# Kernel tuning notes

Hardware: AMD Instinct MI355X
Metric: run time of the kernel (lower is better)

Reference implementation:

```python
import jax, jax.numpy as jnp
import numpy as np

N, D, H, E = 50000, 64, 4, 400000
LN_EPS = 1e-5


def setup_inputs() -> dict:
    key = jax.random.key(0)
    ks = jax.random.split(key, 8)
    x = jax.random.normal(ks[0], (N, D), dtype=jnp.float32)
    edge_index = jax.random.randint(ks[1], (2, E), 0, N, dtype=jnp.int64)
    # nn.Linear(dim, dim*heads, bias=False): weight shape (H*D, D)
    W_lin = jax.random.normal(ks[2], (H * D, D), dtype=jnp.float32) * (1.0 / np.sqrt(D))
    attn_src = jax.random.normal(ks[3], (H, D), dtype=jnp.float32) * 0.1
    attn_dst = jax.random.normal(ks[4], (H, D), dtype=jnp.float32) * 0.1
    # nn.Linear(dim*heads, dim): weight (D, H*D), bias (D,)
    W_out = jax.random.normal(ks[5], (D, H * D), dtype=jnp.float32) * (1.0 / np.sqrt(H * D))
    b_out = jnp.zeros((D,), dtype=jnp.float32)
    ln_g = jnp.ones((D,), dtype=jnp.float32)
    ln_b = jnp.zeros((D,), dtype=jnp.float32)
    return {"x": x, "edge_index": edge_index, "W_lin": W_lin,
            "attn_src": attn_src, "attn_dst": attn_dst,
            "W_out": W_out, "b_out": b_out, "ln_g": ln_g, "ln_b": ln_b}


def reference(x, edge_index, W_lin, attn_src, attn_dst, W_out, b_out, ln_g, ln_b):
    n = x.shape[0]
    i, j = edge_index[0], edge_index[1]  # dst, src node ids per edge
    xh = (x @ W_lin.T).reshape(n, H, D)                 # [N,H,D]
    # per-node attention contributions (equivalent to per-edge dot in source)
    s_dst = jnp.einsum('nhd,hd->nh', xh, attn_dst)      # [N,H]
    s_src = jnp.einsum('nhd,hd->nh', xh, attn_src)      # [N,H]
    alpha = jax.nn.leaky_relu(s_dst[i] + s_src[j], 0.2) # [E,H]
    alpha_exp = jnp.exp(alpha)                          # source uses raw exp (no max-shift)
    denom = jax.ops.segment_sum(alpha_exp, i, num_segments=n)  # [N,H]
    attn = alpha_exp / (denom[i] + 1e-9)                # [E,H]
    msg = attn[:, :, None] * xh[j]                      # [E,H,D]
    out = jax.ops.segment_sum(msg, i, num_segments=n)   # [N,H,D]
    out = out.reshape(n, H * D) @ W_out.T + b_out       # [N,D]
    y = jax.nn.elu(out) + x
    mu = jnp.mean(y, axis=-1, keepdims=True)
    var = jnp.mean(jnp.square(y - mu), axis=-1, keepdims=True)
    return (y - mu) * jax.lax.rsqrt(var + LN_EPS) * ln_g + ln_b
```

## Files before the change

### kernel.cpp

```cpp
#include <hip/hip_runtime.h>

#define N_NODES 50000
#define DIM     64
#define HEADS   4
#define NEDGES  400000
#define HD      256
#define MAXDEG  32
#define NTILES  3125

typedef _Float16 half4v __attribute__((ext_vector_type(4)));
typedef _Float16 half8v __attribute__((ext_vector_type(8)));
typedef float    f32x4  __attribute__((ext_vector_type(4)));

union EU { int2 i2; half4v h; };

__global__ __launch_bounds__(256) void k_wG(
    const float* __restrict__ W_lin,
    const float* __restrict__ attn_src,
    const float* __restrict__ attn_dst,
    const float* __restrict__ W_out,
    _Float16* __restrict__ G2T,
    float* __restrict__ weff,
    int* __restrict__ cnt)
{
    const int b = blockIdx.x;
    const int t = threadIdx.x;

    for (int idx = b * 256 + t; idx < N_NODES; idx += 65 * 256)
        cnt[idx] = 0;

    if (b < 64) {
        const int id = b * 256 + t;
        const int d = id >> 8, rem = id & 255, m = rem >> 2, h = rem & 3;
        float acc = 0.f;
        for (int k = 0; k < DIM; ++k)
            acc = fmaf(W_lin[(h * DIM + k) * DIM + m], W_out[d * HD + h * DIM + k], acc);
        G2T[d * HD + m * 4 + h] = (_Float16)acc;
    } else {
        for (int id = t; id < 512; id += 256) {
            const int sd = id >> 8, rem = id & 255, h = rem >> 6, k = rem & 63;
            const float* av = sd ? attn_dst : attn_src;
            float acc = 0.f;
            for (int d = 0; d < DIM; ++d)
                acc = fmaf(av[h * DIM + d], W_lin[(h * DIM + d) * DIM + k], acc);
            weff[(sd * 4 + h) * DIM + k] = acc;
        }
    }
}

__global__ __launch_bounds__(256) void k_xS(
    const float* __restrict__ x,
    const float* __restrict__ weff,
    _Float16* __restrict__ x16,
    float* __restrict__ S)
{
    const int t = threadIdx.x;
    const int base = blockIdx.x * 32;

    const int ni = base + (t >> 3);
    if (ni < N_NODES) {
        const int combo = t & 7;
        const float4* xr = (const float4*)(x + (size_t)ni * DIM);
        const float4* wr = (const float4*)(weff + combo * DIM);
        float acc = 0.f;
#pragma unroll
        for (int kp = 0; kp < 16; ++kp) {
            const float4 a = xr[kp], bw = wr[kp];
            acc = fmaf(a.x, bw.x, acc);
            acc = fmaf(a.y, bw.y, acc);
            acc = fmaf(a.z, bw.z, acc);
            acc = fmaf(a.w, bw.w, acc);
        }
        S[(size_t)ni * 8 + combo] = acc;
    }

    const size_t e0 = (size_t)base * DIM + (size_t)t * 8;
    if (e0 + 8 <= (size_t)N_NODES * DIM) {
        const float4 u = *(const float4*)(x + e0);
        const float4 v = *(const float4*)(x + e0 + 4);
        half8v hv;
        hv[0]=(_Float16)u.x; hv[1]=(_Float16)u.y; hv[2]=(_Float16)u.z; hv[3]=(_Float16)u.w;
        hv[4]=(_Float16)v.x; hv[5]=(_Float16)v.y; hv[6]=(_Float16)v.z; hv[7]=(_Float16)v.w;
        *(half8v*)(x16 + e0) = hv;
    }
}

__global__ __launch_bounds__(256) void k_edge(
    const int* __restrict__ ei,
    const float* __restrict__ S,
    int* __restrict__ cnt,
    int4* __restrict__ bucketE)
{
    const int e = blockIdx.x * 256 + threadIdx.x;
    if (e >= NEDGES) return;
    const int i = ei[e];
    const int j = ei[NEDGES + e];
    const float4 sd = *(const float4*)(S + (size_t)i * 8 + 4);
    const float4 ss = *(const float4*)(S + (size_t)j * 8);
    float u;
    u = sd.x + ss.x; u = u > 0.f ? u : 0.2f * u; const float e0 = __expf(u);
    u = sd.y + ss.y; u = u > 0.f ? u : 0.2f * u; const float e1 = __expf(u);
    u = sd.z + ss.z; u = u > 0.f ? u : 0.2f * u; const float e2 = __expf(u);
    u = sd.w + ss.w; u = u > 0.f ? u : 0.2f * u; const float e3 = __expf(u);
    EU pk;
    pk.h[0] = (_Float16)e0; pk.h[1] = (_Float16)e1;
    pk.h[2] = (_Float16)e2; pk.h[3] = (_Float16)e3;
    int4 ent;
    ent.x = j; ent.y = pk.i2.x; ent.z = pk.i2.y; ent.w = 0;
    const int slot = atomicAdd(&cnt[i], 1);
    if (slot < MAXDEG) bucketE[(size_t)i * MAXDEG + slot] = ent;
}

__global__ __launch_bounds__(256) void k_gather(
    const int* __restrict__ cnt,
    const int4* __restrict__ bucketE,
    const _Float16* __restrict__ x16,
    _Float16* __restrict__ zn)
{
    const int t = threadIdx.x;
    const int wv = t >> 6, l = t & 63;
    const int n = blockIdx.x * 4 + wv;

    const int dg = cnt[n];
    const int deg = dg < MAXDEG ? dg : MAXDEG;
    const int4 E = bucketE[(size_t)n * MAXDEG + (l & 31)];

    float z0 = 0.f, z1 = 0.f, z2 = 0.f, z3 = 0.f;
    float d0 = 0.f, d1 = 0.f, d2 = 0.f, d3 = 0.f;

    for (int s = 0; s < deg; s += 4) {
        int jj[4], ey[4], ez[4];
#pragma unroll
        for (int q = 0; q < 4; ++q) {
            const int ss = s + q;
            const int jv = __shfl(E.x, ss, 64);
            const int yv = __shfl(E.y, ss, 64);
            const int zv = __shfl(E.z, ss, 64);
            const bool v = ss < deg;
            jj[q] = v ? jv : 0;
            ey[q] = v ? yv : 0;
            ez[q] = v ? zv : 0;
        }
        float xv[4];
#pragma unroll
        for (int q = 0; q < 4; ++q)
            xv[q] = (float)x16[(size_t)jj[q] * DIM + l];
#pragma unroll
        for (int q = 0; q < 4; ++q) {
            EU u; u.i2 = make_int2(ey[q], ez[q]);
            const float e0 = (float)u.h[0], e1 = (float)u.h[1];
            const float e2 = (float)u.h[2], e3 = (float)u.h[3];
            d0 += e0; d1 += e1; d2 += e2; d3 += e3;
            z0 = fmaf(e0, xv[q], z0);
            z1 = fmaf(e1, xv[q], z1);
            z2 = fmaf(e2, xv[q], z2);
            z3 = fmaf(e3, xv[q], z3);
        }
    }

    half4v o;
    o[0] = (_Float16)(z0 / (d0 + 1e-9f));
    o[1] = (_Float16)(z1 / (d1 + 1e-9f));
    o[2] = (_Float16)(z2 / (d2 + 1e-9f));
    o[3] = (_Float16)(z3 / (d3 + 1e-9f));
    *(half4v*)(zn + (size_t)n * HD + l * 4) = o;
}

__global__ __launch_bounds__(256) void k_out(
    const _Float16* __restrict__ zn,
    const _Float16* __restrict__ G2T,
    const float* __restrict__ b_out,
    const float* __restrict__ ln_g,
    const float* __restrict__ ln_b,
    const float* __restrict__ x,
    float* __restrict__ out)
{
    const int wv = threadIdx.x >> 6, l = threadIdx.x & 63;
    const int tile = blockIdx.x * 4 + wv;
    if (tile >= NTILES) return;
    const int n0 = tile * 16;
    const int mrow = l & 15, quad = l >> 4;

    half8v A[8];
    const _Float16* zr = zn + (size_t)(n0 + mrow) * HD + quad * 8;
#pragma unroll
    for (int s = 0; s < 8; ++s)
        A[s] = *(const half8v*)(zr + 32 * s);

    f32x4 acc[4];
#pragma unroll
    for (int tt = 0; tt < 4; ++tt) {
        const _Float16* gp = G2T + (size_t)(tt * 16 + mrow) * HD + quad * 8;
        f32x4 c = {0.f, 0.f, 0.f, 0.f};
#pragma unroll
        for (int s = 0; s < 8; ++s)
            c = __builtin_amdgcn_mfma_f32_16x16x32_f16(A[s], *(const half8v*)(gp + 32 * s), c, 0, 0, 0);
        acc[tt] = c;
    }

    float bo[4], lg[4], lb[4];
#pragma unroll
    for (int tt = 0; tt < 4; ++tt) {
        const int c = tt * 16 + mrow;
        bo[tt] = b_out[c]; lg[tt] = ln_g[c]; lb[tt] = ln_b[c];
    }

#pragma unroll
    for (int rho = 0; rho < 4; ++rho) {
        const int node = n0 + quad * 4 + rho;
        float y[4];
#pragma unroll
        for (int tt = 0; tt < 4; ++tt) {
            const float o = acc[tt][rho] + bo[tt];
            const float eo = o > 0.f ? o : expm1f(o);
            y[tt] = eo + x[(size_t)node * DIM + tt * 16 + mrow];
        }
        float s4 = y[0] + y[1] + y[2] + y[3];
#pragma unroll
        for (int off = 8; off > 0; off >>= 1) s4 += __shfl_xor(s4, off, 64);
        const float mu = s4 * (1.f / 64.f);
        float vs = 0.f;
#pragma unroll
        for (int tt = 0; tt < 4; ++tt) {
            const float dd = y[tt] - mu;
            vs = fmaf(dd, dd, vs);
        }
#pragma unroll
        for (int off = 8; off > 0; off >>= 1) vs += __shfl_xor(vs, off, 64);
        const float r = rsqrtf(vs * (1.f / 64.f) + 1e-5f);
#pragma unroll
        for (int tt = 0; tt < 4; ++tt)
            out[(size_t)node * DIM + tt * 16 + mrow] = (y[tt] - mu) * r * lg[tt] + lb[tt];
    }
}

extern "C" void kernel_launch(void* const* d_in, const int* in_sizes, int n_in,
                              void* d_out, int out_size, void* d_ws, size_t ws_size,
                              hipStream_t stream)
{
    const float* x        = (const float*)d_in[0];
    const int*   ei       = (const int*)d_in[1];
    const float* W_lin    = (const float*)d_in[2];
    const float* attn_src = (const float*)d_in[3];
    const float* attn_dst = (const float*)d_in[4];
    const float* W_out    = (const float*)d_in[5];
    const float* b_out    = (const float*)d_in[6];
    const float* ln_g     = (const float*)d_in[7];
    const float* ln_b     = (const float*)d_in[8];
    float* out = (float*)d_out;

    char* ws = (char*)d_ws;
    _Float16* zn     = (_Float16*)ws;
    _Float16* x16    = zn + (size_t)N_NODES * HD;
    float*    S      = (float*)(x16 + (size_t)N_NODES * DIM);
    _Float16* G2T    = (_Float16*)(S + (size_t)N_NODES * 8);
    float*    weff   = (float*)(G2T + 64 * HD);
    int*      cnt    = (int*)(weff + 512);
    int4*     bucketE= (int4*)(cnt + N_NODES);

    k_wG<<<65, 256, 0, stream>>>(W_lin, attn_src, attn_dst, W_out,
                                 G2T, weff, cnt);

    k_xS<<<(N_NODES + 31) / 32, 256, 0, stream>>>(x, weff, x16, S);

    k_edge<<<(NEDGES + 255) / 256, 256, 0, stream>>>(ei, S, cnt, bucketE);

    k_gather<<<N_NODES / 4, 256, 0, stream>>>(cnt, bucketE, x16, zn);

    k_out<<<(NTILES + 3) / 4, 256, 0, stream>>>(zn, G2T, b_out, ln_g, ln_b, x, out);
}
```

Baseline: 174.4 us.

## Fuse gather with output projection and merge weight prep with x conversion

```diff
diff --git a/kernel.cpp b/kernel.cpp
--- a/kernel.cpp
+++ b/kernel.cpp
@@ -6,7 +6,8 @@
 #define NEDGES  400000
 #define HD      256
 #define MAXDEG  32
-#define NTILES  3125
+#define NPREP   200
+#define ZSTRIDE 264
 
 typedef _Float16 half4v __attribute__((ext_vector_type(4)));
 typedef _Float16 half8v __attribute__((ext_vector_type(8)));
@@ -14,74 +15,71 @@
 
 union EU { int2 i2; half4v h; };
 
-__global__ __launch_bounds__(256) void k_wG(
+__global__ __launch_bounds__(256) void k_prep(
+    const float* __restrict__ x,
     const float* __restrict__ W_lin,
     const float* __restrict__ attn_src,
     const float* __restrict__ attn_dst,
     const float* __restrict__ W_out,
     _Float16* __restrict__ G2T,
-    float* __restrict__ weff,
+    _Float16* __restrict__ x16,
+    float* __restrict__ S,
     int* __restrict__ cnt)
 {
-    const int b = blockIdx.x;
-    const int t = threadIdx.x;
-
-    for (int idx = b * 256 + t; idx < N_NODES; idx += 65 * 256)
+    __shared__ float weffsh[512];
+    const int b = blockIdx.x, t = threadIdx.x;
+
+    for (int id = t; id < 512; id += 256) {
+        const int sd = id >> 8, rem = id & 255, h = rem >> 6, k = rem & 63;
+        const float* av = sd ? attn_dst : attn_src;
+        float acc = 0.f;
+        for (int d = 0; d < DIM; ++d)
+            acc = fmaf(av[h * DIM + d], W_lin[(h * DIM + d) * DIM + k], acc);
+        weffsh[id] = acc;
+    }
+
+    for (int idx = b * 256 + t; idx < N_NODES; idx += NPREP * 256)
         cnt[idx] = 0;
 
-    if (b < 64) {
+    {
         const int id = b * 256 + t;
-        const int d = id >> 8, rem = id & 255, m = rem >> 2, h = rem & 3;
-        float acc = 0.f;
-        for (int k = 0; k < DIM; ++k)
-            acc = fmaf(W_lin[(h * DIM + k) * DIM + m], W_out[d * HD + h * DIM + k], acc);
-        G2T[d * HD + m * 4 + h] = (_Float16)acc;
-    } else {
-        for (int id = t; id < 512; id += 256) {
-            const int sd = id >> 8, rem = id & 255, h = rem >> 6, k = rem & 63;
-            const float* av = sd ? attn_dst : attn_src;
+        if (id < 64 * 256) {
+            const int d = id >> 8, rem = id & 255, m = rem >> 2, h = rem & 3;
             float acc = 0.f;
-            for (int d = 0; d < DIM; ++d)
-                acc = fmaf(av[h * DIM + d], W_lin[(h * DIM + d) * DIM + k], acc);
-            weff[(sd * 4 + h) * DIM + k] = acc;
-        }
-    }
-}
-
-__global__ __launch_bounds__(256) void k_xS(
-    const float* __restrict__ x,
-    const float* __restrict__ weff,
-    _Float16* __restrict__ x16,
-    float* __restrict__ S)
-{
-    const int t = threadIdx.x;
-    const int base = blockIdx.x * 32;
-
-    const int ni = base + (t >> 3);
-    if (ni < N_NODES) {
-        const int combo = t & 7;
-        const float4* xr = (const float4*)(x + (size_t)ni * DIM);
-        const float4* wr = (const float4*)(weff + combo * DIM);
-        float acc = 0.f;
-#pragma unroll
-        for (int kp = 0; kp < 16; ++kp) {
-            const float4 a = xr[kp], bw = wr[kp];
-            acc = fmaf(a.x, bw.x, acc);
-            acc = fmaf(a.y, bw.y, acc);
-            acc = fmaf(a.z, bw.z, acc);
-            acc = fmaf(a.w, bw.w, acc);
-        }
-        S[(size_t)ni * 8 + combo] = acc;
-    }
-
-    const size_t e0 = (size_t)base * DIM + (size_t)t * 8;
-    if (e0 + 8 <= (size_t)N_NODES * DIM) {
-        const float4 u = *(const float4*)(x + e0);
-        const float4 v = *(const float4*)(x + e0 + 4);
-        half8v hv;
-        hv[0]=(_Float16)u.x; hv[1]=(_Float16)u.y; hv[2]=(_Float16)u.z; hv[3]=(_Float16)u.w;
-        hv[4]=(_Float16)v.x; hv[5]=(_Float16)v.y; hv[6]=(_Float16)v.z; hv[7]=(_Float16)v.w;
-        *(half8v*)(x16 + e0) = hv;
+            for (int k = 0; k < DIM; ++k)
+                acc = fmaf(W_lin[(h * DIM + k) * DIM + m],
+                           W_out[d * HD + h * DIM + k], acc);
+            G2T[d * HD + m * 4 + h] = (_Float16)acc;
+        }
+    }
+    __syncthreads();
+
+    for (int base = b * 32; base < N_NODES; base += NPREP * 32) {
+        const int ni = base + (t >> 3);
+        if (ni < N_NODES) {
+            const int combo = t & 7;
+            const float4* xr = (const float4*)(x + (size_t)ni * DIM);
+            const float4* wr = (const float4*)(weffsh + combo * DIM);
+            float acc = 0.f;
+#pragma unroll
+            for (int kp = 0; kp < 16; ++kp) {
+                const float4 a = xr[kp], bw = wr[kp];
+                acc = fmaf(a.x, bw.x, acc);
+                acc = fmaf(a.y, bw.y, acc);
+                acc = fmaf(a.z, bw.z, acc);
+                acc = fmaf(a.w, bw.w, acc);
+            }
+            S[(size_t)ni * 8 + combo] = acc;
+        }
+        const size_t e0 = (size_t)base * DIM + (size_t)t * 8;
+        if (e0 + 8 <= (size_t)N_NODES * DIM) {
+            const float4 u = *(const float4*)(x + e0);
+            const float4 v = *(const float4*)(x + e0 + 4);
+            half8v hv;
+            hv[0]=(_Float16)u.x; hv[1]=(_Float16)u.y; hv[2]=(_Float16)u.z; hv[3]=(_Float16)u.w;
+            hv[4]=(_Float16)v.x; hv[5]=(_Float16)v.y; hv[6]=(_Float16)v.z; hv[7]=(_Float16)v.w;
+            *(half8v*)(x16 + e0) = hv;
+        }
     }
 }
 
@@ -111,63 +109,10 @@
     if (slot < MAXDEG) bucketE[(size_t)i * MAXDEG + slot] = ent;
 }
 
-__global__ __launch_bounds__(256) void k_gather(
+__global__ __launch_bounds__(256) void k_ga(
     const int* __restrict__ cnt,
     const int4* __restrict__ bucketE,
     const _Float16* __restrict__ x16,
-    _Float16* __restrict__ zn)
-{
-    const int t = threadIdx.x;
-    const int wv = t >> 6, l = t & 63;
-    const int n = blockIdx.x * 4 + wv;
-
-    const int dg = cnt[n];
-    const int deg = dg < MAXDEG ? dg : MAXDEG;
-    const int4 E = bucketE[(size_t)n * MAXDEG + (l & 31)];
-
-    float z0 = 0.f, z1 = 0.f, z2 = 0.f, z3 = 0.f;
-    float d0 = 0.f, d1 = 0.f, d2 = 0.f, d3 = 0.f;
-
-    for (int s = 0; s < deg; s += 4) {
-        int jj[4], ey[4], ez[4];
-#pragma unroll
-        for (int q = 0; q < 4; ++q) {
-            const int ss = s + q;
-            const int jv = __shfl(E.x, ss, 64);
-            const int yv = __shfl(E.y, ss, 64);
-            const int zv = __shfl(E.z, ss, 64);
-            const bool v = ss < deg;
-            jj[q] = v ? jv : 0;
-            ey[q] = v ? yv : 0;
-            ez[q] = v ? zv : 0;
-        }
-        float xv[4];
-#pragma unroll
-        for (int q = 0; q < 4; ++q)
-            xv[q] = (float)x16[(size_t)jj[q] * DIM + l];
-#pragma unroll
-        for (int q = 0; q < 4; ++q) {
-            EU u; u.i2 = make_int2(ey[q], ez[q]);
-            const float e0 = (float)u.h[0], e1 = (float)u.h[1];
-            const float e2 = (float)u.h[2], e3 = (float)u.h[3];
-            d0 += e0; d1 += e1; d2 += e2; d3 += e3;
-            z0 = fmaf(e0, xv[q], z0);
-            z1 = fmaf(e1, xv[q], z1);
-            z2 = fmaf(e2, xv[q], z2);
-            z3 = fmaf(e3, xv[q], z3);
-        }
-    }
-
-    half4v o;
-    o[0] = (_Float16)(z0 / (d0 + 1e-9f));
-    o[1] = (_Float16)(z1 / (d1 + 1e-9f));
-    o[2] = (_Float16)(z2 / (d2 + 1e-9f));
-    o[3] = (_Float16)(z3 / (d3 + 1e-9f));
-    *(half4v*)(zn + (size_t)n * HD + l * 4) = o;
-}
-
-__global__ __launch_bounds__(256) void k_out(
-    const _Float16* __restrict__ zn,
     const _Float16* __restrict__ G2T,
     const float* __restrict__ b_out,
     const float* __restrict__ ln_g,
@@ -175,62 +120,98 @@
     const float* __restrict__ x,
     float* __restrict__ out)
 {
-    const int wv = threadIdx.x >> 6, l = threadIdx.x & 63;
-    const int tile = blockIdx.x * 4 + wv;
-    if (tile >= NTILES) return;
-    const int n0 = tile * 16;
+    __shared__ _Float16 znsh[16 * ZSTRIDE];
+    __shared__ float ysh[16][65];
+
+    const int t = threadIdx.x, wv = t >> 6, l = t & 63;
+    const int n0 = blockIdx.x * 16;
+
+    for (int r = 0; r < 4; ++r) {
+        const int n = n0 + wv * 4 + r;
+        const int dg = cnt[n];
+        const int deg = dg < MAXDEG ? dg : MAXDEG;
+        const int4 E = bucketE[(size_t)n * MAXDEG + (l & 31)];
+
+        float z0 = 0.f, z1 = 0.f, z2 = 0.f, z3 = 0.f;
+        float d0 = 0.f, d1 = 0.f, d2 = 0.f, d3 = 0.f;
+
+        for (int s = 0; s < deg; s += 4) {
+            int jj[4], ey[4], ez[4];
+#pragma unroll
+            for (int q = 0; q < 4; ++q) {
+                const int ss = s + q;
+                const int jv = __shfl(E.x, ss, 64);
+                const int yv = __shfl(E.y, ss, 64);
+                const int zv = __shfl(E.z, ss, 64);
+                const bool v = ss < deg;
+                jj[q] = v ? jv : 0;
+                ey[q] = v ? yv : 0;
+                ez[q] = v ? zv : 0;
+            }
+            float xv[4];
+#pragma unroll
+            for (int q = 0; q < 4; ++q)
+                xv[q] = (float)x16[(size_t)jj[q] * DIM + l];
+#pragma unroll
+            for (int q = 0; q < 4; ++q) {
+                EU u; u.i2 = make_int2(ey[q], ez[q]);
+                const float e0 = (float)u.h[0], e1 = (float)u.h[1];
+                const float e2 = (float)u.h[2], e3 = (float)u.h[3];
+                d0 += e0; d1 += e1; d2 += e2; d3 += e3;
+                z0 = fmaf(e0, xv[q], z0);
+                z1 = fmaf(e1, xv[q], z1);
+                z2 = fmaf(e2, xv[q], z2);
+                z3 = fmaf(e3, xv[q], z3);
+            }
+        }
+        half4v o;
+        o[0] = (_Float16)(z0 / (d0 + 1e-9f));
+        o[1] = (_Float16)(z1 / (d1 + 1e-9f));
+        o[2] = (_Float16)(z2 / (d2 + 1e-9f));
+        o[3] = (_Float16)(z3 / (d3 + 1e-9f));
+        *(half4v*)(znsh + (wv * 4 + r) * ZSTRIDE + l * 4) = o;
+    }
+    __syncthreads();
+
     const int mrow = l & 15, quad = l >> 4;
-
     half8v A[8];
-    const _Float16* zr = zn + (size_t)(n0 + mrow) * HD + quad * 8;
+    const _Float16* zr = znsh + mrow * ZSTRIDE + quad * 8;
 #pragma unroll
     for (int s = 0; s < 8; ++s)
         A[s] = *(const half8v*)(zr + 32 * s);
 
-    f32x4 acc[4];
-#pragma unroll
-    for (int tt = 0; tt < 4; ++tt) {
-        const _Float16* gp = G2T + (size_t)(tt * 16 + mrow) * HD + quad * 8;
-        f32x4 c = {0.f, 0.f, 0.f, 0.f};
-#pragma unroll
-        for (int s = 0; s < 8; ++s)
-            c = __builtin_amdgcn_mfma_f32_16x16x32_f16(A[s], *(const half8v*)(gp + 32 * s), c, 0, 0, 0);
-        acc[tt] = c;
-    }
-
-    float bo[4], lg[4], lb[4];
-#pragma unroll
-    for (int tt = 0; tt < 4; ++tt) {
-        const int c = tt * 16 + mrow;
-        bo[tt] = b_out[c]; lg[tt] = ln_g[c]; lb[tt] = ln_b[c];
-    }
-
+    const _Float16* gp = G2T + (size_t)(wv * 16 + mrow) * HD + quad * 8;
+    f32x4 c = {0.f, 0.f, 0.f, 0.f};
+#pragma unroll
+    for (int s = 0; s < 8; ++s)
+        c = __builtin_amdgcn_mfma_f32_16x16x32_f16(A[s], *(const half8v*)(gp + 32 * s), c, 0, 0, 0);
+
+    const int col = wv * 16 + mrow;
+    const float bo = b_out[col];
 #pragma unroll
     for (int rho = 0; rho < 4; ++rho) {
-        const int node = n0 + quad * 4 + rho;
-        float y[4];
-#pragma unroll
-        for (int tt = 0; tt < 4; ++tt) {
-            const float o = acc[tt][rho] + bo[tt];
-            const float eo = o > 0.f ? o : expm1f(o);
-            y[tt] = eo + x[(size_t)node * DIM + tt * 16 + mrow];
-        }
-        float s4 = y[0] + y[1] + y[2] + y[3];
-#pragma unroll
-        for (int off = 8; off > 0; off >>= 1) s4 += __shfl_xor(s4, off, 64);
-        const float mu = s4 * (1.f / 64.f);
-        float vs = 0.f;
-#pragma unroll
-        for (int tt = 0; tt < 4; ++tt) {
-            const float dd = y[tt] - mu;
-            vs = fmaf(dd, dd, vs);
-        }
-#pragma unroll
-        for (int off = 8; off > 0; off >>= 1) vs += __shfl_xor(vs, off, 64);
-        const float r = rsqrtf(vs * (1.f / 64.f) + 1e-5f);
-#pragma unroll
-        for (int tt = 0; tt < 4; ++tt)
-            out[(size_t)node * DIM + tt * 16 + mrow] = (y[tt] - mu) * r * lg[tt] + lb[tt];
+        const int nl = quad * 4 + rho;
+        const float o = c[rho] + bo;
+        const float eo = o > 0.f ? o : expm1f(o);
+        ysh[nl][col] = eo + x[(size_t)(n0 + nl) * DIM + col];
+    }
+    __syncthreads();
+
+    const float g = ln_g[l], bb = ln_b[l];
+#pragma unroll
+    for (int r = 0; r < 4; ++r) {
+        const int nl = wv * 4 + r;
+        const float y = ysh[nl][l];
+        float sum = y;
+#pragma unroll
+        for (int off = 32; off > 0; off >>= 1) sum += __shfl_xor(sum, off, 64);
+        const float mu = sum * (1.f / 64.f);
+        const float dy = y - mu;
+        float vs = dy * dy;
+#pragma unroll
+        for (int off = 32; off > 0; off >>= 1) vs += __shfl_xor(vs, off, 64);
+        const float rr = rsqrtf(vs * (1.f / 64.f) + 1e-5f);
+        out[(size_t)(n0 + nl) * DIM + l] = dy * rr * g + bb;
     }
 }
 
@@ -250,22 +231,17 @@
     float* out = (float*)d_out;
 
     char* ws = (char*)d_ws;
-    _Float16* zn     = (_Float16*)ws;
-    _Float16* x16    = zn + (size_t)N_NODES * HD;
+    _Float16* x16    = (_Float16*)ws;
     float*    S      = (float*)(x16 + (size_t)N_NODES * DIM);
     _Float16* G2T    = (_Float16*)(S + (size_t)N_NODES * 8);
-    float*    weff   = (float*)(G2T + 64 * HD);
-    int*      cnt    = (int*)(weff + 512);
+    int*      cnt    = (int*)(G2T + 64 * HD);
     int4*     bucketE= (int4*)(cnt + N_NODES);
 
-    k_wG<<<65, 256, 0, stream>>>(W_lin, attn_src, attn_dst, W_out,
-                                 G2T, weff, cnt);
-
-    k_xS<<<(N_NODES + 31) / 32, 256, 0, stream>>>(x, weff, x16, S);
+    k_prep<<<NPREP, 256, 0, stream>>>(x, W_lin, attn_src, attn_dst, W_out,
+                                      G2T, x16, S, cnt);
 
     k_edge<<<(NEDGES + 255) / 256, 256, 0, stream>>>(ei, S, cnt, bucketE);
 
-    k_gather<<<N_NODES / 4, 256, 0, stream>>>(cnt, bucketE, x16, zn);
-
-    k_out<<<(NTILES + 3) / 4, 256, 0, stream>>>(zn, G2T, b_out, ln_g, ln_b, x, out);
-}
+    k_ga<<<N_NODES / 16, 256, 0, stream>>>(cnt, bucketE, x16, G2T,
+                                           b_out, ln_g, ln_b, x, out);
+}
```

Measured after the change: 164.0 us. 5.9% less time.
